# Kernel optimization log

Measured on AMD Instinct MI355X. Metric: run time of the kernel, lower is better.

## Reference

```python
import jax, jax.numpy as jnp
import numpy as np
import math

N_HEAD = 16
H_DIM = 64  # (n_dim // n_head) // 2
LAMBDA_INIT = 0.8 - 0.6 * math.exp(-0.3 * 1)  # depth = 1


def setup_inputs() -> dict:
    key = jax.random.key(0)
    ks = jax.random.split(key, 7)
    B, T, C = 1, 2048, 2048
    std = 0.02
    return {
        "x": jax.random.normal(ks[0], (B, T, C), jnp.float32),
        "w_qkv": jax.random.normal(ks[1], (C, 3 * C), jnp.float32) * std,
        "w_proj": jax.random.normal(ks[2], (C, C), jnp.float32) * std,
        "lambda_q1": jax.random.normal(ks[3], (H_DIM,), jnp.float32) * 0.1,
        "lambda_k1": jax.random.normal(ks[4], (H_DIM,), jnp.float32) * 0.1,
        "lambda_q2": jax.random.normal(ks[5], (H_DIM,), jnp.float32) * 0.1,
        "lambda_k2": jax.random.normal(ks[6], (H_DIM,), jnp.float32) * 0.1,
        "rms_scale": jnp.ones((2 * H_DIM,), jnp.float32),
    }


def _sdpa(q, k, v, scale):
    # q,k: [B,H,T,d]; v: [B,H,T,2d]
    scores = jnp.einsum("bhqd,bhkd->bhqk", q, k) * scale
    probs = jax.nn.softmax(scores, axis=-1)
    return jnp.einsum("bhqk,bhkd->bhqd", probs, v)


def reference(x, w_qkv, w_proj, lambda_q1, lambda_k1, lambda_q2, lambda_k2, rms_scale):
    B, T, C = x.shape
    qkv = x @ w_qkv  # [B,T,3C]
    q, k, v = jnp.split(qkv, 3, axis=-1)
    # q,k -> [B, 2*n_head, T, h_dim]; v -> [B, n_head, T, 2*h_dim]
    q = q.reshape(B, T, 2 * N_HEAD, H_DIM).transpose(0, 2, 1, 3)
    k = k.reshape(B, T, 2 * N_HEAD, H_DIM).transpose(0, 2, 1, 3)
    v = v.reshape(B, T, N_HEAD, 2 * H_DIM).transpose(0, 2, 1, 3)
    q1, q2 = q[:, :N_HEAD], q[:, N_HEAD:]
    k1, k2 = k[:, :N_HEAD], k[:, N_HEAD:]
    scale = 1.0 / math.sqrt(H_DIM)
    a1 = _sdpa(q1, k1, v, scale)  # [B,H,T,2*h_dim]
    a2 = _sdpa(q2, k2, v, scale)
    lam1 = jnp.exp(jnp.sum(lambda_q1 * lambda_k1))
    lam2 = jnp.exp(jnp.sum(lambda_q2 * lambda_k2))
    lam = lam1 - lam2 + LAMBDA_INIT
    out = a1 - lam * a2
    # per-head RMSNorm over last dim (2*h_dim), fp32
    o32 = out.astype(jnp.float32)
    normed = o32 * jax.lax.rsqrt(jnp.mean(o32 * o32, axis=-1, keepdims=True) + 1e-6)
    out = (normed.astype(out.dtype) * rms_scale) * (1.0 - LAMBDA_INIT)
    out = out.transpose(0, 2, 1, 3).reshape(B, T, C)
    return out @ w_proj
```

## Files before the change

### kernel.cpp

```cpp
#include <hip/hip_runtime.h>


typedef unsigned short u16;
typedef __attribute__((ext_vector_type(8))) short bf16x8;
typedef __attribute__((ext_vector_type(4))) float f32x4;

#define MFMA16(a, b, c) __builtin_amdgcn_mfma_f32_16x16x32_bf16((a), (b), (c), 0, 0, 0)

#define LAMBDA_INIT_F 0.35550906759096926f
#define ONE_MINUS_LI_F 0.64449093240903074f
#define QSCALE 0.18033688011112042f
#define DEFER_THR 11.541560327111707f

__device__ __forceinline__ u16 f2bf(float f) {
  union { float f; unsigned u; } v; v.f = f;
  unsigned r = v.u + 0x7fffu + ((v.u >> 16) & 1u);
  return (u16)(r >> 16);
}
__device__ __forceinline__ u16 fastbf(float f) {
  union { float f; unsigned u; } v; v.f = f;
  return (u16)((v.u + 0x8000u) >> 16);
}
__device__ __forceinline__ float bf2f(u16 h) {
  union { unsigned u; float f; } v; v.u = ((unsigned)h) << 16;
  return v.f;
}
__device__ __forceinline__ int sw3(int row) { return (row & 3) << 3; }
__device__ __forceinline__ int sw7(int row) { return (row & 7) << 3; }
__device__ __forceinline__ float fexp2(float x) { return __builtin_exp2f(x); }

__device__ __forceinline__ void gload16(const u16* g, u16* l) {
  __builtin_amdgcn_global_load_lds((const __attribute__((address_space(1))) void*)g,
                                   (__attribute__((address_space(3))) void*)l,
                                   16, 0, 0);
}


__global__ void lam_kernel(const float* __restrict__ q1, const float* __restrict__ k1,
                           const float* __restrict__ q2, const float* __restrict__ k2,
                           float* __restrict__ out) {
  int l = threadIdx.x;
  float p1 = q1[l] * k1[l];
  float p2 = q2[l] * k2[l];
#pragma unroll
  for (int m = 32; m >= 1; m >>= 1) {
    p1 += __shfl_xor(p1, m, 64);
    p2 += __shfl_xor(p2, m, 64);
  }
  if (l == 0) out[0] = expf(p1) - expf(p2) + LAMBDA_INIT_F;
}

__global__ void split_x_kernel(const float* __restrict__ X, u16* __restrict__ H,
                               u16* __restrict__ L) {
  int idx = blockIdx.x * 256 + threadIdx.x;
  int t = idx >> 9;
  int c0 = (idx & 511) << 2;
  float4 v = *reinterpret_cast<const float4*>(X + ((size_t)t << 11) + c0);
  float vv[4] = {v.x, v.y, v.z, v.w};
  int s = sw3(t);
  size_t base = (size_t)t << 11;
#pragma unroll
  for (int j = 0; j < 4; ++j) {
    int c = (c0 + j) ^ s;
    u16 h = f2bf(vv[j]);
    H[base + c] = h;
    L[base + c] = f2bf(vv[j] - bf2f(h));
  }
}

__global__ void transpose_kernel(const float* __restrict__ W, u16* __restrict__ TH, int K,
                                 int N) {
  __shared__ float tile[64][65];
  int bk = blockIdx.x * 64, bn = blockIdx.y * 64;
  for (int i = threadIdx.x; i < 64 * 64; i += 256) {
    int r = i >> 6, c = i & 63;
    tile[r][c] = W[(size_t)(bk + r) * N + bn + c];
  }
  __syncthreads();
  for (int i = threadIdx.x; i < 64 * 64; i += 256) {
    int r = i >> 6, c = i & 63;
    float v = tile[c][r];
    int n = bn + r, k = bk + c;
    TH[(size_t)n * K + (k ^ sw3(n))] = f2bf(v);
  }
}

template <int EPI, int BM>
__global__ __launch_bounds__(256, 3) void gemm_bf16x2(
    const u16* __restrict__ Agh, const u16* __restrict__ Agl, const u16* __restrict__ Bgh,
    int N, int K, u16* __restrict__ qk_h, u16* __restrict__ vt_h, float* __restrict__ outp) {
  constexpr int AC = BM / 16;
  constexpr int CPW = (2 * AC + 8) / 4;
  constexpr int ASZ = BM * 32;
  constexpr int MR = BM / 32;
  __shared__ __align__(16) u16 LA[(2 * BM + 128) * 32];
  const int tid = threadIdx.x;
  const int w = tid >> 6, lane = tid & 63;
  const int lr = lane & 15, kg = lane >> 4;
  const int bn0 = blockIdx.x * 128, bm0 = blockIdx.y * BM;
  const int wm = (w >> 1) * (BM / 2), wn = (w & 1) * 64;
  const int srow = lane >> 2, scol = (lane & 3) << 3;

  f32x4 acc[MR][4];
  const f32x4 VZ = {0.f, 0.f, 0.f, 0.f};
#pragma unroll
  for (int m = 0; m < MR; ++m)
#pragma unroll
    for (int n = 0; n < 4; ++n) acc[m][n] = VZ;

  for (int k0 = 0; k0 < K; k0 += 32) {
    __syncthreads();
#pragma unroll
    for (int j = 0; j < CPW; ++j) {
      int i = w * CPW + j;
      int a = (i < AC) ? 0 : (i < 2 * AC) ? 1 : 2;
      int c = i - ((a == 0) ? 0 : (a == 1) ? AC : 2 * AC);
      const u16* src = (a == 0) ? Agh : (a == 1) ? Agl : Bgh;
      int tb = (a < 2) ? bm0 : bn0;
      gload16(src + (size_t)(tb + c * 16 + srow) * K + k0 + scol, &LA[a * ASZ + c * 512]);
    }
    __syncthreads();

    bf16x8 ah[MR], al[MR], bh[4];
#pragma unroll
    for (int m = 0; m < MR; ++m) {
      int row = wm + m * 16 + lr;
      int off = (row << 5) + ((kg << 3) ^ sw3(row));
      ah[m] = *reinterpret_cast<const bf16x8*>(&LA[0] + off);
      al[m] = *reinterpret_cast<const bf16x8*>(&LA[ASZ] + off);
    }
#pragma unroll
    for (int n = 0; n < 4; ++n) {
      int row = wn + n * 16 + lr;
      int off = (row << 5) + ((kg << 3) ^ sw3(row));
      bh[n] = *reinterpret_cast<const bf16x8*>(&LA[2 * ASZ] + off);
    }
#pragma unroll
    for (int m = 0; m < MR; ++m)
#pragma unroll
      for (int n = 0; n < 4; ++n) {
        acc[m][n] = MFMA16(ah[m], bh[n], acc[m][n]);
        acc[m][n] = MFMA16(al[m], bh[n], acc[m][n]);
      }
  }

#pragma unroll
  for (int m = 0; m < MR; ++m) {
#pragma unroll
    for (int n = 0; n < 4; ++n) {
#pragma unroll
      for (int r = 0; r < 4; ++r) {
        int row = bm0 + wm + m * 16 + (kg << 2) + r;
        int col = bn0 + wn + n * 16 + lr;
        float v = acc[m][n][r];
        if (EPI == 0) {
          if (col < 2048) v *= QSCALE;
          u16 hh = f2bf(v);
          if (col < 4096) {
            int cc = (col < 2048) ? col : (2048 + ((col - 2048) ^ sw7(row)));
            qk_h[((size_t)row << 12) + cc] = hh;
          } else {
            int vc = col - 4096;
            vt_h[((size_t)vc << 11) + (row ^ sw7(vc))] = hh;
          }
        } else {
          outp[(size_t)row * N + col] = v;
        }
      }
    }
  }
}

__global__ __launch_bounds__(256, 2) void diff_attn_kernel(
    const u16* __restrict__ qk_h, const u16* __restrict__ vt_h, const float* __restrict__ lam_p,
    const float* __restrict__ rms_scale, u16* __restrict__ at_h, u16* __restrict__ at_l) {
  __shared__ __align__(16) u16 KL[2][64][64];
  __shared__ __align__(16) u16 VL[128][64];
  __shared__ __align__(16) u16 PL[4][2][16][64];

  const int tid = threadIdx.x;
  const int w = tid >> 6, lane = tid & 63;
  const int lr = lane & 15, kg = lane >> 4;
  const int h = blockIdx.y;
  const int qb = blockIdx.x * 64 + w * 16;
  const float lam = lam_p[0];
  const f32x4 VZ = {0.f, 0.f, 0.f, 0.f};
  const bf16x8 ONES = {0x3f80, 0x3f80, 0x3f80, 0x3f80, 0x3f80, 0x3f80, 0x3f80, 0x3f80};

  bf16x8 qf[2][2];
  {
    const size_t qrb = ((size_t)(qb + lr)) << 12;
#pragma unroll
    for (int s = 0; s < 2; ++s) {
      int qo = h * 64 + s * 1024;
#pragma unroll
      for (int kc = 0; kc < 2; ++kc)
        qf[s][kc] = *reinterpret_cast<const bf16x8*>(qk_h + qrb + qo + kc * 32 + (kg << 3));
    }
  }

  f32x4 o1[8], o2[8];
#pragma unroll
  for (int n = 0; n < 8; ++n) { o1[n] = VZ; o2[n] = VZ; }
  float m[4], l1[4], l2[4];
#pragma unroll
  for (int r = 0; r < 4; ++r) { m[r] = -1e30f; l1[r] = l2[r] = 0.f; }

  const int srow8 = lane >> 3, scol8 = (lane & 7) << 3;
  const int koff = 2048 + h * 64 + w * 1024;

  for (int kt = 0; kt < 2048; kt += 64) {
    __syncthreads();
    if (w < 2) {
#pragma unroll
      for (int c = 0; c < 8; ++c)
        gload16(qk_h + (((size_t)(kt + c * 8 + srow8)) << 12) + koff + scol8, &KL[w][c * 8][0]);
    } else {
      const int vb = (w - 2) * 64;
#pragma unroll
      for (int c = 0; c < 8; ++c)
        gload16(vt_h + (((size_t)(h * 128 + vb + c * 8 + srow8)) << 11) + kt + scol8,
                &VL[vb + c * 8][0]);
    }
    __syncthreads();

    f32x4 s1[4], s2[4];
#pragma unroll
    for (int n = 0; n < 4; ++n) { s1[n] = VZ; s2[n] = VZ; }
#pragma unroll
    for (int n = 0; n < 4; ++n) {
      int key = n * 16 + lr;
#pragma unroll
      for (int kc = 0; kc < 2; ++kc) {
        int off = (key << 6) + (((kc << 5) + (kg << 3)) ^ sw7(key));
        bf16x8 k1 = *reinterpret_cast<const bf16x8*>(&KL[0][0][0] + off);
        bf16x8 k2 = *reinterpret_cast<const bf16x8*>(&KL[1][0][0] + off);
        s1[n] = MFMA16(qf[0][kc], k1, s1[n]);
        s2[n] = MFMA16(qf[1][kc], k2, s2[n]);
      }
    }

    float tmax[4];
#pragma unroll
    for (int r = 0; r < 4; ++r) {
      float t = fmaxf(fmaxf(fmaxf(s1[0][r], s1[1][r]), fmaxf(s1[2][r], s1[3][r])),
                      fmaxf(fmaxf(s2[0][r], s2[1][r]), fmaxf(s2[2][r], s2[3][r])));
      t = fmaxf(t, __shfl_xor(t, 1, 64));
      t = fmaxf(t, __shfl_xor(t, 2, 64));
      t = fmaxf(t, __shfl_xor(t, 4, 64));
      t = fmaxf(t, __shfl_xor(t, 8, 64));
      tmax[r] = t;
    }
    int need = 0;
#pragma unroll
    for (int r = 0; r < 4; ++r) need |= (tmax[r] > m[r] + DEFER_THR) ? 1 : 0;
    if (__any(need)) {
#pragma unroll
      for (int r = 0; r < 4; ++r) {
        float mn = fmaxf(m[r], tmax[r]);
        float corr = fexp2(m[r] - mn);
        m[r] = mn;
        l1[r] *= corr;
        l2[r] *= corr;
#pragma unroll
        for (int n = 0; n < 8; ++n) { o1[n][r] *= corr; o2[n][r] *= corr; }
      }
    }
#pragma unroll
    for (int n = 0; n < 4; ++n)
#pragma unroll
      for (int r = 0; r < 4; ++r) {
        float p1 = fexp2(s1[n][r] - m[r]);
        float p2 = fexp2(s2[n][r] - m[r]);
        int qp = (n * 2 + (lr >> 3) + kg + 2 * r) & 7;
        int idx = qp * 8 + (lr & 7);
        PL[w][0][4 * kg + r][idx] = fastbf(p1);
        PL[w][1][4 * kg + r][idx] = fastbf(p2);
      }

    bf16x8 pa1[2], pa2[2];
#pragma unroll
    for (int ks = 0; ks < 2; ++ks) {
      int qp = (ks * 4 + kg + (lr >> 2) + 2 * (lr & 3)) & 7;
      pa1[ks] = *reinterpret_cast<const bf16x8*>(&PL[w][0][lr][qp * 8]);
      pa2[ks] = *reinterpret_cast<const bf16x8*>(&PL[w][1][lr][qp * 8]);
    }
    f32x4 lacc1 = MFMA16(pa1[1], ONES, MFMA16(pa1[0], ONES, VZ));
    f32x4 lacc2 = MFMA16(pa2[1], ONES, MFMA16(pa2[0], ONES, VZ));
#pragma unroll
    for (int r = 0; r < 4; ++r) { l1[r] += lacc1[r]; l2[r] += lacc2[r]; }

#pragma unroll
    for (int n = 0; n < 8; ++n) {
      int vd = n * 16 + lr;
#pragma unroll
      for (int ks = 0; ks < 2; ++ks) {
        int off = (vd << 6) + (((ks << 5) + (kg << 3)) ^ sw7(vd));
        bf16x8 vf = *reinterpret_cast<const bf16x8*>(&VL[0][0] + off);
        o1[n] = MFMA16(pa1[ks], vf, o1[n]);
        o2[n] = MFMA16(pa2[ks], vf, o2[n]);
      }
    }
  }

  float nsc[4];
  {
    float il1[4], il2[4], ss[4];
#pragma unroll
    for (int r = 0; r < 4; ++r) { il1[r] = 1.f / l1[r]; il2[r] = 1.f / l2[r]; ss[r] = 0.f; }
#pragma unroll
    for (int n = 0; n < 8; ++n)
#pragma unroll
      for (int r = 0; r < 4; ++r) {
        float v = o1[n][r] * il1[r] - lam * (o2[n][r] * il2[r]);
        o1[n][r] = v;
        ss[r] += v * v;
      }
#pragma unroll
    for (int r = 0; r < 4; ++r) {
      float t = ss[r];
      t += __shfl_xor(t, 1, 64);
      t += __shfl_xor(t, 2, 64);
      t += __shfl_xor(t, 4, 64);
      t += __shfl_xor(t, 8, 64);
      nsc[r] = rsqrtf(t * (1.f / 128.f) + 1e-6f) * ONE_MINUS_LI_F;
    }
  }
#pragma unroll
  for (int n = 0; n < 8; ++n) {
    float rs = rms_scale[n * 16 + lr];
#pragma unroll
    for (int r = 0; r < 4; ++r) {
      int row = qb + (kg << 2) + r;
      int col = h * 128 + n * 16 + lr;
      float v = o1[n][r] * nsc[r] * rs;
      u16 hh = f2bf(v);
      int cc = col ^ sw3(row);
      at_h[((size_t)row << 11) + cc] = hh;
      at_l[((size_t)row << 11) + cc] = f2bf(v - bf2f(hh));
    }
  }
}


extern "C" void kernel_launch(void* const* d_in, const int* in_sizes, int n_in, void* d_out,
                              int out_size, void* d_ws, size_t ws_size, hipStream_t stream) {
  (void)in_sizes; (void)n_in; (void)out_size;
  const float* x = (const float*)d_in[0];
  const float* wqkv = (const float*)d_in[1];
  const float* wprj = (const float*)d_in[2];
  const float* lq1 = (const float*)d_in[3];
  const float* lk1 = (const float*)d_in[4];
  const float* lq2 = (const float*)d_in[5];
  const float* lk2 = (const float*)d_in[6];
  const float* rms = (const float*)d_in[7];
  float* out = (float*)d_out;

  char* p = (char*)d_ws;
  auto take = [&](size_t n) { char* r = p; p += (n + 255) & ~(size_t)255; return r; };
  float* lam = (float*)take(256);
  u16* x_h = (u16*)take(2048ull * 2048 * 2);
  u16* x_l = (u16*)take(2048ull * 2048 * 2);
  u16* wqT_h = (u16*)take(6144ull * 2048 * 2);
  u16* wpT_h = (u16*)take(2048ull * 2048 * 2);
  u16* qk_h = (u16*)take(2048ull * 4096 * 2);
  u16* vt_h = (u16*)take(2048ull * 2048 * 2);
  u16* at_h = (u16*)take(2048ull * 2048 * 2);
  u16* at_l = (u16*)take(2048ull * 2048 * 2);
  if ((size_t)(p - (char*)d_ws) > ws_size) return;

  lam_kernel<<<1, 64, 0, stream>>>(lq1, lk1, lq2, lk2, lam);
  split_x_kernel<<<4096, 256, 0, stream>>>(x, x_h, x_l);
  transpose_kernel<<<dim3(32, 96), 256, 0, stream>>>(wqkv, wqT_h, 2048, 6144);
  transpose_kernel<<<dim3(32, 32), 256, 0, stream>>>(wprj, wpT_h, 2048, 2048);

  gemm_bf16x2<0, 128><<<dim3(48, 16), 256, 0, stream>>>(x_h, x_l, wqT_h, 6144, 2048, qk_h,
                                                        vt_h, nullptr);
  diff_attn_kernel<<<dim3(32, 16), 256, 0, stream>>>(qk_h, vt_h, lam, rms, at_h, at_l);
  gemm_bf16x2<1, 64><<<dim3(16, 32), 256, 0, stream>>>(at_h, at_l, wpT_h, 2048, 2048, nullptr,
                                                       nullptr, out);
}
```

Measured before the change: 391.5 us.

## Double K-step depth in GEMM and attention tiles, add MFMA priority hints

The GEMM now stages 64-wide K slices per iteration instead of 32, with the swizzle widened from 3 to 7 bits across the producer kernels to match the 128-byte rows. The attention kernel processes 128 keys per iteration instead of 64, with larger K/V LDS tiles, and splits the P·V step into two halves. It also wraps the MFMA sections in s_setprio. The aim is to halve barrier and loop overhead per unit of work. In exchange, LDS use roughly doubles, GEMM occupancy drops from 3 to 2 blocks per CU, and register pressure rises from the wider score arrays.

Result: faster. 354.7 us (-9.4%).

```diff
diff --git a/kernel.cpp b/kernel.cpp
--- a/kernel.cpp
+++ b/kernel.cpp
@@ -25,7 +25,6 @@
   union { unsigned u; float f; } v; v.u = ((unsigned)h) << 16;
   return v.f;
 }
-__device__ __forceinline__ int sw3(int row) { return (row & 3) << 3; }
 __device__ __forceinline__ int sw7(int row) { return (row & 7) << 3; }
 __device__ __forceinline__ float fexp2(float x) { return __builtin_exp2f(x); }
 
@@ -57,7 +56,7 @@
   int c0 = (idx & 511) << 2;
   float4 v = *reinterpret_cast<const float4*>(X + ((size_t)t << 11) + c0);
   float vv[4] = {v.x, v.y, v.z, v.w};
-  int s = sw3(t);
+  int s = sw7(t);
   size_t base = (size_t)t << 11;
 #pragma unroll
   for (int j = 0; j < 4; ++j) {
@@ -81,25 +80,26 @@
     int r = i >> 6, c = i & 63;
     float v = tile[c][r];
     int n = bn + r, k = bk + c;
-    TH[(size_t)n * K + (k ^ sw3(n))] = f2bf(v);
+    TH[(size_t)n * K + (k ^ sw7(n))] = f2bf(v);
   }
 }
 
 template <int EPI, int BM>
-__global__ __launch_bounds__(256, 3) void gemm_bf16x2(
+__global__ __launch_bounds__(256, 2) void gemm_bf16x2(
     const u16* __restrict__ Agh, const u16* __restrict__ Agl, const u16* __restrict__ Bgh,
     int N, int K, u16* __restrict__ qk_h, u16* __restrict__ vt_h, float* __restrict__ outp) {
-  constexpr int AC = BM / 16;
-  constexpr int CPW = (2 * AC + 8) / 4;
-  constexpr int ASZ = BM * 32;
+  constexpr int ACH = BM / 8;
+  constexpr int NCH = 2 * ACH + 16;
+  constexpr int CPW = NCH / 4;
+  constexpr int ASZ = BM * 64;
   constexpr int MR = BM / 32;
-  __shared__ __align__(16) u16 LA[(2 * BM + 128) * 32];
+  __shared__ __align__(16) u16 LA[(2 * BM + 128) * 64];
   const int tid = threadIdx.x;
   const int w = tid >> 6, lane = tid & 63;
   const int lr = lane & 15, kg = lane >> 4;
   const int bn0 = blockIdx.x * 128, bm0 = blockIdx.y * BM;
   const int wm = (w >> 1) * (BM / 2), wn = (w & 1) * 64;
-  const int srow = lane >> 2, scol = (lane & 3) << 3;
+  const int srow = lane >> 3, scol = (lane & 7) << 3;
 
   f32x4 acc[MR][4];
   const f32x4 VZ = {0.f, 0.f, 0.f, 0.f};
@@ -108,40 +108,43 @@
 #pragma unroll
     for (int n = 0; n < 4; ++n) acc[m][n] = VZ;
 
-  for (int k0 = 0; k0 < K; k0 += 32) {
+  for (int k0 = 0; k0 < K; k0 += 64) {
     __syncthreads();
 #pragma unroll
     for (int j = 0; j < CPW; ++j) {
       int i = w * CPW + j;
-      int a = (i < AC) ? 0 : (i < 2 * AC) ? 1 : 2;
-      int c = i - ((a == 0) ? 0 : (a == 1) ? AC : 2 * AC);
+      int a = (i < ACH) ? 0 : (i < 2 * ACH) ? 1 : 2;
+      int c = i - ((a == 0) ? 0 : (a == 1) ? ACH : 2 * ACH);
       const u16* src = (a == 0) ? Agh : (a == 1) ? Agl : Bgh;
       int tb = (a < 2) ? bm0 : bn0;
-      gload16(src + (size_t)(tb + c * 16 + srow) * K + k0 + scol, &LA[a * ASZ + c * 512]);
+      gload16(src + (size_t)(tb + c * 8 + srow) * K + k0 + scol, &LA[a * ASZ + c * 512]);
     }
     __syncthreads();
 
-    bf16x8 ah[MR], al[MR], bh[4];
-#pragma unroll
-    for (int m = 0; m < MR; ++m) {
-      int row = wm + m * 16 + lr;
-      int off = (row << 5) + ((kg << 3) ^ sw3(row));
-      ah[m] = *reinterpret_cast<const bf16x8*>(&LA[0] + off);
-      al[m] = *reinterpret_cast<const bf16x8*>(&LA[ASZ] + off);
-    }
-#pragma unroll
-    for (int n = 0; n < 4; ++n) {
-      int row = wn + n * 16 + lr;
-      int off = (row << 5) + ((kg << 3) ^ sw3(row));
-      bh[n] = *reinterpret_cast<const bf16x8*>(&LA[2 * ASZ] + off);
-    }
-#pragma unroll
-    for (int m = 0; m < MR; ++m)
+#pragma unroll
+    for (int kc = 0; kc < 2; ++kc) {
+      bf16x8 ah[MR], al[MR], bh[4];
+#pragma unroll
+      for (int m = 0; m < MR; ++m) {
+        int row = wm + m * 16 + lr;
+        int off = (row << 6) + (((kc << 5) | (kg << 3)) ^ sw7(row));
+        ah[m] = *reinterpret_cast<const bf16x8*>(&LA[0] + off);
+        al[m] = *reinterpret_cast<const bf16x8*>(&LA[ASZ] + off);
+      }
 #pragma unroll
       for (int n = 0; n < 4; ++n) {
-        acc[m][n] = MFMA16(ah[m], bh[n], acc[m][n]);
-        acc[m][n] = MFMA16(al[m], bh[n], acc[m][n]);
-      }
+        int row = wn + n * 16 + lr;
+        int off = (row << 6) + (((kc << 5) | (kg << 3)) ^ sw7(row));
+        bh[n] = *reinterpret_cast<const bf16x8*>(&LA[2 * ASZ] + off);
+      }
+#pragma unroll
+      for (int m = 0; m < MR; ++m)
+#pragma unroll
+        for (int n = 0; n < 4; ++n) {
+          acc[m][n] = MFMA16(ah[m], bh[n], acc[m][n]);
+          acc[m][n] = MFMA16(al[m], bh[n], acc[m][n]);
+        }
+    }
   }
 
 #pragma unroll
@@ -174,8 +177,8 @@
 __global__ __launch_bounds__(256, 2) void diff_attn_kernel(
     const u16* __restrict__ qk_h, const u16* __restrict__ vt_h, const float* __restrict__ lam_p,
     const float* __restrict__ rms_scale, u16* __restrict__ at_h, u16* __restrict__ at_l) {
-  __shared__ __align__(16) u16 KL[2][64][64];
-  __shared__ __align__(16) u16 VL[128][64];
+  __shared__ __align__(16) u16 KL[2][128][64];
+  __shared__ __align__(16) u16 VL[128][128];
   __shared__ __align__(16) u16 PL[4][2][16][64];
 
   const int tid = threadIdx.x;
@@ -207,44 +210,51 @@
   for (int r = 0; r < 4; ++r) { m[r] = -1e30f; l1[r] = l2[r] = 0.f; }
 
   const int srow8 = lane >> 3, scol8 = (lane & 7) << 3;
+  const int srow4 = lane >> 4, scol4 = (lane & 15) << 3;
   const int koff = 2048 + h * 64 + w * 1024;
 
-  for (int kt = 0; kt < 2048; kt += 64) {
+  for (int kt = 0; kt < 2048; kt += 128) {
     __syncthreads();
     if (w < 2) {
 #pragma unroll
-      for (int c = 0; c < 8; ++c)
-        gload16(qk_h + (((size_t)(kt + c * 8 + srow8)) << 12) + koff + scol8, &KL[w][c * 8][0]);
+      for (int c = 0; c < 16; ++c)
+        gload16(qk_h + (((size_t)(kt + c * 8 + srow8)) << 12) + koff + scol8,
+                &KL[w][c * 8][0]);
     } else {
       const int vb = (w - 2) * 64;
 #pragma unroll
-      for (int c = 0; c < 8; ++c)
-        gload16(vt_h + (((size_t)(h * 128 + vb + c * 8 + srow8)) << 11) + kt + scol8,
-                &VL[vb + c * 8][0]);
+      for (int c = 0; c < 16; ++c)
+        gload16(vt_h + (((size_t)(h * 128 + vb + c * 4 + srow4)) << 11) + kt + scol4,
+                &VL[vb + c * 4][0]);
     }
     __syncthreads();
 
-    f32x4 s1[4], s2[4];
-#pragma unroll
-    for (int n = 0; n < 4; ++n) { s1[n] = VZ; s2[n] = VZ; }
-#pragma unroll
-    for (int n = 0; n < 4; ++n) {
+    f32x4 s1[8], s2[8];
+#pragma unroll
+    for (int n = 0; n < 8; ++n) { s1[n] = VZ; s2[n] = VZ; }
+    __builtin_amdgcn_s_setprio(1);
+#pragma unroll
+    for (int n = 0; n < 8; ++n) {
       int key = n * 16 + lr;
 #pragma unroll
       for (int kc = 0; kc < 2; ++kc) {
-        int off = (key << 6) + (((kc << 5) + (kg << 3)) ^ sw7(key));
+        int off = (key << 6) + (((kc << 5) | (kg << 3)) ^ sw7(key));
         bf16x8 k1 = *reinterpret_cast<const bf16x8*>(&KL[0][0][0] + off);
         bf16x8 k2 = *reinterpret_cast<const bf16x8*>(&KL[1][0][0] + off);
         s1[n] = MFMA16(qf[0][kc], k1, s1[n]);
         s2[n] = MFMA16(qf[1][kc], k2, s2[n]);
       }
     }
+    __builtin_amdgcn_s_setprio(0);
 
     float tmax[4];
 #pragma unroll
     for (int r = 0; r < 4; ++r) {
       float t = fmaxf(fmaxf(fmaxf(s1[0][r], s1[1][r]), fmaxf(s1[2][r], s1[3][r])),
-                      fmaxf(fmaxf(s2[0][r], s2[1][r]), fmaxf(s2[2][r], s2[3][r])));
+                      fmaxf(fmaxf(s1[4][r], s1[5][r]), fmaxf(s1[6][r], s1[7][r])));
+      float t2 = fmaxf(fmaxf(fmaxf(s2[0][r], s2[1][r]), fmaxf(s2[2][r], s2[3][r])),
+                       fmaxf(fmaxf(s2[4][r], s2[5][r]), fmaxf(s2[6][r], s2[7][r])));
+      t = fmaxf(t, t2);
       t = fmaxf(t, __shfl_xor(t, 1, 64));
       t = fmaxf(t, __shfl_xor(t, 2, 64));
       t = fmaxf(t, __shfl_xor(t, 4, 64));
@@ -266,40 +276,47 @@
         for (int n = 0; n < 8; ++n) { o1[n][r] *= corr; o2[n][r] *= corr; }
       }
     }
-#pragma unroll
-    for (int n = 0; n < 4; ++n)
-#pragma unroll
-      for (int r = 0; r < 4; ++r) {
-        float p1 = fexp2(s1[n][r] - m[r]);
-        float p2 = fexp2(s2[n][r] - m[r]);
-        int qp = (n * 2 + (lr >> 3) + kg + 2 * r) & 7;
-        int idx = qp * 8 + (lr & 7);
-        PL[w][0][4 * kg + r][idx] = fastbf(p1);
-        PL[w][1][4 * kg + r][idx] = fastbf(p2);
-      }
-
-    bf16x8 pa1[2], pa2[2];
-#pragma unroll
-    for (int ks = 0; ks < 2; ++ks) {
-      int qp = (ks * 4 + kg + (lr >> 2) + 2 * (lr & 3)) & 7;
-      pa1[ks] = *reinterpret_cast<const bf16x8*>(&PL[w][0][lr][qp * 8]);
-      pa2[ks] = *reinterpret_cast<const bf16x8*>(&PL[w][1][lr][qp * 8]);
-    }
-    f32x4 lacc1 = MFMA16(pa1[1], ONES, MFMA16(pa1[0], ONES, VZ));
-    f32x4 lacc2 = MFMA16(pa2[1], ONES, MFMA16(pa2[0], ONES, VZ));
-#pragma unroll
-    for (int r = 0; r < 4; ++r) { l1[r] += lacc1[r]; l2[r] += lacc2[r]; }
-
-#pragma unroll
-    for (int n = 0; n < 8; ++n) {
-      int vd = n * 16 + lr;
+
+#pragma unroll
+    for (int hs = 0; hs < 2; ++hs) {
+#pragma unroll
+      for (int nn = 0; nn < 4; ++nn) {
+        int n = hs * 4 + nn;
+#pragma unroll
+        for (int r = 0; r < 4; ++r) {
+          float p1 = fexp2(s1[n][r] - m[r]);
+          float p2 = fexp2(s2[n][r] - m[r]);
+          int qp = (nn * 2 + (lr >> 3) + kg + 2 * r) & 7;
+          int idx = qp * 8 + (lr & 7);
+          PL[w][0][4 * kg + r][idx] = fastbf(p1);
+          PL[w][1][4 * kg + r][idx] = fastbf(p2);
+        }
+      }
+      bf16x8 pa1[2], pa2[2];
 #pragma unroll
       for (int ks = 0; ks < 2; ++ks) {
-        int off = (vd << 6) + (((ks << 5) + (kg << 3)) ^ sw7(vd));
-        bf16x8 vf = *reinterpret_cast<const bf16x8*>(&VL[0][0] + off);
-        o1[n] = MFMA16(pa1[ks], vf, o1[n]);
-        o2[n] = MFMA16(pa2[ks], vf, o2[n]);
-      }
+        int qp = (ks * 4 + kg + (lr >> 2) + 2 * (lr & 3)) & 7;
+        pa1[ks] = *reinterpret_cast<const bf16x8*>(&PL[w][0][lr][qp * 8]);
+        pa2[ks] = *reinterpret_cast<const bf16x8*>(&PL[w][1][lr][qp * 8]);
+      }
+      f32x4 lacc1 = MFMA16(pa1[1], ONES, MFMA16(pa1[0], ONES, VZ));
+      f32x4 lacc2 = MFMA16(pa2[1], ONES, MFMA16(pa2[0], ONES, VZ));
+#pragma unroll
+      for (int r = 0; r < 4; ++r) { l1[r] += lacc1[r]; l2[r] += lacc2[r]; }
+
+      __builtin_amdgcn_s_setprio(1);
+#pragma unroll
+      for (int n = 0; n < 8; ++n) {
+        int vd = n * 16 + lr;
+#pragma unroll
+        for (int ks = 0; ks < 2; ++ks) {
+          int off = (vd << 7) + ((((hs * 2 + ks) << 5) | (kg << 3)) ^ sw7(vd));
+          bf16x8 vf = *reinterpret_cast<const bf16x8*>(&VL[0][0] + off);
+          o1[n] = MFMA16(pa1[ks], vf, o1[n]);
+          o2[n] = MFMA16(pa2[ks], vf, o2[n]);
+        }
+      }
+      __builtin_amdgcn_s_setprio(0);
     }
   }
 
@@ -335,7 +352,7 @@
       int col = h * 128 + n * 16 + lr;
       float v = o1[n][r] * nsc[r] * rs;
       u16 hh = f2bf(v);
-      int cc = col ^ sw3(row);
+      int cc = col ^ sw7(row);
       at_h[((size_t)row << 11) + cc] = hh;
       at_l[((size_t)row << 11) + cc] = f2bf(v - bf2f(hh));
     }
```
